# Performance work log

Hardware: AMD Instinct MI355X
Metric: run time of the kernel (lower is better)

Reference implementation:

```python
import jax, jax.numpy as jnp
import numpy as np

N_NODES = 50000
N_EDGES = 800000
IN_DIM = 128
HID_DIM = 64
OUT_DIM = 64
NUM_GRAPHS = 512


def setup_inputs() -> dict:
    key = jax.random.key(0)
    ks = jax.random.split(key, 8)
    x = jax.random.normal(ks[0], (N_NODES, IN_DIM), dtype=jnp.float32)
    edge_index = jax.random.randint(ks[1], (2, N_EDGES), 0, N_NODES, dtype=jnp.int64)
    batch = jnp.sort(jax.random.randint(ks[2], (N_NODES,), 0, NUM_GRAPHS, dtype=jnp.int64))
    s1 = 1.0 / np.sqrt(IN_DIM)
    s2 = 1.0 / np.sqrt(HID_DIM)
    W1 = jax.random.uniform(ks[3], (IN_DIM, HID_DIM), jnp.float32, -s1, s1)
    b1 = jax.random.uniform(ks[4], (HID_DIM,), jnp.float32, -s1, s1)
    W2 = jax.random.uniform(ks[5], (HID_DIM, OUT_DIM), jnp.float32, -s2, s2)
    b2 = jax.random.uniform(ks[6], (OUT_DIM,), jnp.float32, -s2, s2)
    return {"x": x, "edge_index": edge_index, "batch": batch,
            "W1": W1, "b1": b1, "W2": W2, "b2": b2}


def _gcn_layer(h, W, b, src, dst, norm, n_nodes):
    # linear transform first (keeps the per-edge gather at output width)
    h = h @ W + b                      # [N, d_out]
    msg = h[src] * norm[:, None]       # [E, d_out] gathered, normalized messages
    agg = jax.ops.segment_sum(msg, dst, num_segments=n_nodes)  # scatter-add
    return jax.nn.relu(agg)


def reference(x, edge_index, batch, W1, b1, W2, b2):
    src, dst = edge_index[0], edge_index[1]
    # symmetric degree normalization: deg^{-1/2}[src] * deg^{-1/2}[dst]
    deg = jax.ops.segment_sum(jnp.ones((src.shape[0],), x.dtype), dst,
                              num_segments=N_NODES)
    dinv = jax.lax.rsqrt(jnp.maximum(deg, 1.0))
    norm = dinv[src] * dinv[dst]       # [E]

    h = _gcn_layer(x, W1, b1, src, dst, norm, N_NODES)   # dropout = identity (eval)
    h = _gcn_layer(h, W2, b2, src, dst, norm, N_NODES)

    # scatter_mean pooling over batch indices
    sums = jax.ops.segment_sum(h, batch, num_segments=NUM_GRAPHS)
    cnts = jax.ops.segment_sum(jnp.ones((N_NODES,), h.dtype), batch,
                               num_segments=NUM_GRAPHS)
    return sums / jnp.maximum(cnts, 1.0)[:, None]        # [NUM_GRAPHS, OUT_DIM]
```

## Files before the change

kernel.cpp:

```cpp
#include <hip/hip_runtime.h>
#include <hip/hip_fp16.h>

#define N_NODES 50000
#define N_EDGES 800000
#define IN_DIM 128
#define NUM_GRAPHS 512
#define CAP 64
#define NB 196
#define BCAP 5120
#define FILL_T 2048
#define NFILL 391
#define GEMM_TILES 1563

typedef unsigned short u16;
typedef unsigned int u32;

__device__ __forceinline__ void acc_row(const uint4& v, float2& aa, float2& ab,
                                        float2& ac, float2& ad) {
    const __half2* hp = reinterpret_cast<const __half2*>(&v);
    float2 f;
    f = __half22float2(hp[0]); aa.x += f.x; aa.y += f.y;
    f = __half22float2(hp[1]); ab.x += f.x; ab.y += f.y;
    f = __half22float2(hp[2]); ac.x += f.x; ac.y += f.y;
    f = __half22float2(hp[3]); ad.x += f.x; ad.y += f.y;
}

__device__ __forceinline__ void gather_node(
    const uint4* __restrict__ H16, const u16* __restrict__ sp, int dg, int lo,
    float2& aa, float2& ab, float2& ac, float2& ad) {
    int i = 0;
    for (; i + 7 < dg; i += 8) {
        ushort4 s4a = *reinterpret_cast<const ushort4*>(sp + i);
        ushort4 s4b = *reinterpret_cast<const ushort4*>(sp + i + 4);
        uint4 v0 = H16[(size_t)s4a.x * 8 + lo];
        uint4 v1 = H16[(size_t)s4a.y * 8 + lo];
        uint4 v2 = H16[(size_t)s4a.z * 8 + lo];
        uint4 v3 = H16[(size_t)s4a.w * 8 + lo];
        uint4 v4 = H16[(size_t)s4b.x * 8 + lo];
        uint4 v5 = H16[(size_t)s4b.y * 8 + lo];
        uint4 v6 = H16[(size_t)s4b.z * 8 + lo];
        uint4 v7 = H16[(size_t)s4b.w * 8 + lo];
        acc_row(v0, aa, ab, ac, ad); acc_row(v1, aa, ab, ac, ad);
        acc_row(v2, aa, ab, ac, ad); acc_row(v3, aa, ab, ac, ad);
        acc_row(v4, aa, ab, ac, ad); acc_row(v5, aa, ab, ac, ad);
        acc_row(v6, aa, ab, ac, ad); acc_row(v7, aa, ab, ac, ad);
    }
    for (; i + 3 < dg; i += 4) {
        ushort4 s4 = *reinterpret_cast<const ushort4*>(sp + i);
        uint4 v0 = H16[(size_t)s4.x * 8 + lo];
        uint4 v1 = H16[(size_t)s4.y * 8 + lo];
        uint4 v2 = H16[(size_t)s4.z * 8 + lo];
        uint4 v3 = H16[(size_t)s4.w * 8 + lo];
        acc_row(v0, aa, ab, ac, ad); acc_row(v1, aa, ab, ac, ad);
        acc_row(v2, aa, ab, ac, ad); acc_row(v3, aa, ab, ac, ad);
    }
    for (; i < dg; ++i) {
        uint4 v = H16[(size_t)sp[i] * 8 + lo];
        acc_row(v, aa, ab, ac, ad);
    }
}

__global__ __launch_bounds__(256) void gemm1_fill_kernel(
    const float* __restrict__ X, const float* __restrict__ W,
    const float* __restrict__ bias, __half* __restrict__ Yh, int n_nodes,
    const int* __restrict__ src, const int* __restrict__ dst,
    int* __restrict__ gcursor, u32* __restrict__ packed, int n_edges) {
    __shared__ float xs[32][IN_DIM];
    __shared__ int hist[256], cnt2[256], goffs[256];
    const int tid = threadIdx.x;

    if (blockIdx.x & 1) {
        const int fb = blockIdx.x >> 1;
        if (fb >= NFILL) return;
        hist[tid] = 0; cnt2[tid] = 0;
        __syncthreads();
        const int base = fb * FILL_T;
        int d[8], s[8];
#pragma unroll
        for (int i = 0; i < 8; ++i) {
            int e = base + i * 256 + tid;
            if (e < n_edges) {
                d[i] = dst[e]; s[i] = src[e];
                atomicAdd(&hist[d[i] >> 8], 1);
            } else d[i] = -1;
        }
        __syncthreads();
        if (hist[tid] > 0) goffs[tid] = atomicAdd(&gcursor[tid], hist[tid]);
        __syncthreads();
#pragma unroll
        for (int i = 0; i < 8; ++i) {
            if (d[i] >= 0) {
                int b = d[i] >> 8;
                int p = goffs[b] + atomicAdd(&cnt2[b], 1);
                packed[(size_t)b * BCAP + p] = ((u32)d[i] << 16) | (u32)s[i];
            }
        }
        return;
    }

    const int idx = blockIdx.x >> 1;
    if (idx >= GEMM_TILES) return;
    const int base = idx * 32;
    const int nvec = 32 * IN_DIM / 4;
    const float4* X4 = reinterpret_cast<const float4*>(X + (size_t)base * IN_DIM);
    float4* xs4 = reinterpret_cast<float4*>(&xs[0][0]);
    for (int i = tid; i < nvec; i += 256) {
        int row = i / (IN_DIM / 4);
        xs4[i] = (base + row < n_nodes) ? X4[i] : make_float4(0.f, 0.f, 0.f, 0.f);
    }
    __syncthreads();

    const int j = tid & 63;
    const int w = tid >> 6;
    float b = bias[j];
    float c[8];
#pragma unroll
    for (int r = 0; r < 8; ++r) c[r] = b;
#pragma unroll 4
    for (int k = 0; k < IN_DIM; ++k) {
        float wv = W[k * 64 + j];
#pragma unroll
        for (int r = 0; r < 8; ++r) c[r] += wv * xs[w * 8 + r][k];
    }
    int n0 = base + w * 8;
#pragma unroll
    for (int r = 0; r < 8; ++r)
        if (n0 + r < n_nodes)
            Yh[(size_t)(n0 + r) * 64 + j] = __float2half(c[r]);
}

__global__ __launch_bounds__(256) void fine_kernel(
    const u32* __restrict__ packed, const int* __restrict__ gcursor,
    u16* __restrict__ ssorted, int* __restrict__ deg, float* __restrict__ dinv,
    __half* __restrict__ H1h,
    const int* __restrict__ batch, int* __restrict__ gstart, int n_graphs) {
    __shared__ u16 image[128 * CAP];
    __shared__ int cur[128];
    __shared__ float ds[128];
    const int tid = threadIdx.x;

    if (blockIdx.x == 2 * NB) {
        for (int g = tid; g <= n_graphs; g += 256) {
            int lo = 0, hi = N_NODES;
            while (lo < hi) {
                int mid = (lo + hi) >> 1;
                if (batch[mid] < g) lo = mid + 1; else hi = mid;
            }
            gstart[g] = lo;
        }
        return;
    }

    const int b = blockIdx.x >> 1;
    const int half = blockIdx.x & 1;
    if (tid < 128) cur[tid] = 0;
    __syncthreads();
    const int cnt = gcursor[b];
    const u32* pp = packed + (size_t)b * BCAP;
    for (int i = tid; i < cnt; i += 256) {
        u32 p = pp[i];
        int dl = (p >> 16) & 255;
        if ((dl >> 7) == half) {
            int loc = dl & 127;
            int pos = atomicAdd(&cur[loc], 1);
            if (pos < CAP) image[loc * CAP + pos] = (u16)(p & 0xffff);
        }
    }
    __syncthreads();
    const int nbase = b * 256 + half * 128;
    if (tid < 128) {
        int c = cur[tid];
        float dv = rsqrtf(fmaxf((float)c, 1.0f));
        ds[tid] = dv;
        int d = nbase + tid;
        if (d < N_NODES) { deg[d] = c; dinv[d] = dv; }
    }
    __syncthreads();
    const u32* im32 = reinterpret_cast<const u32*>(image);
    u32* out32 = reinterpret_cast<u32*>(ssorted) + (size_t)nbase * (CAP / 2);
    for (int i = tid; i < 128 * CAP / 2; i += 256) out32[i] = im32[i];
    __half2* Hp = reinterpret_cast<__half2*>(H1h) + (size_t)nbase * 32;
    const int lim = min(128, N_NODES - nbase) * 32;
    for (int i = tid; i < lim; i += 256) {
        float dv = ds[i >> 5];
        float2 f = __half22float2(Hp[i]);
        Hp[i] = __floats2half2_rn(f.x * dv, f.y * dv);
    }
}

__global__ __launch_bounds__(256) void agg_gemm_kernel(
    const __half* __restrict__ H, const u16* __restrict__ ssorted,
    const int* __restrict__ deg, const float* __restrict__ dinv,
    const float* __restrict__ W, const float* __restrict__ bias,
    __half* __restrict__ Yh, int n_nodes) {
    __shared__ float xs[32][64];
    const int tid = threadIdx.x;
    const int lane = tid & 63;
    const int w = tid >> 6;
    const int lo = lane & 7;
    const int slot = w * 8 + (lane >> 3);
    const int base = blockIdx.x * 32;
    const uint4* H16 = reinterpret_cast<const uint4*>(H);

    int node = base + slot;
    float2 aa = make_float2(0.f, 0.f), ab = make_float2(0.f, 0.f);
    float2 ac = make_float2(0.f, 0.f), ad = make_float2(0.f, 0.f);
    if (node < n_nodes) {
        int dg = min(deg[node], CAP);
        gather_node(H16, ssorted + (size_t)node * CAP, dg, lo, aa, ab, ac, ad);
        float dv = dinv[node];
        *reinterpret_cast<float4*>(&xs[slot][8 * lo]) =
            make_float4(fmaxf(aa.x * dv, 0.f), fmaxf(aa.y * dv, 0.f),
                        fmaxf(ab.x * dv, 0.f), fmaxf(ab.y * dv, 0.f));
        *reinterpret_cast<float4*>(&xs[slot][8 * lo + 4]) =
            make_float4(fmaxf(ac.x * dv, 0.f), fmaxf(ac.y * dv, 0.f),
                        fmaxf(ad.x * dv, 0.f), fmaxf(ad.y * dv, 0.f));
    } else {
        *reinterpret_cast<float4*>(&xs[slot][8 * lo]) = make_float4(0.f, 0.f, 0.f, 0.f);
        *reinterpret_cast<float4*>(&xs[slot][8 * lo + 4]) = make_float4(0.f, 0.f, 0.f, 0.f);
    }
    __syncthreads();

    float b = bias[lane];
    float c[8];
#pragma unroll
    for (int r = 0; r < 8; ++r) c[r] = b;
#pragma unroll 4
    for (int k = 0; k < 64; ++k) {
        float wv = W[k * 64 + lane];
#pragma unroll
        for (int r = 0; r < 8; ++r) c[r] += wv * xs[w * 8 + r][k];
    }
    int n0 = base + w * 8;
#pragma unroll
    for (int r = 0; r < 8; ++r)
        if (n0 + r < n_nodes)
            Yh[(size_t)(n0 + r) * 64 + lane] = __float2half(c[r] * dinv[n0 + r]);
}

__global__ __launch_bounds__(512) void agg2_pool_kernel(
    const __half* __restrict__ H, const u16* __restrict__ ssorted,
    const int* __restrict__ deg, const float* __restrict__ dinv,
    const int* __restrict__ gstart, float* __restrict__ out) {
    __shared__ float part[64][64];
    const int g = blockIdx.x;
    const int tid = threadIdx.x;
    const int lane = tid & 63;
    const int w = tid >> 6;
    const int lo = lane & 7;
    const int slot = w * 8 + (lane >> 3);
    const uint4* H16 = reinterpret_cast<const uint4*>(H);
    const int beg = gstart[g], end = gstart[g + 1];

    float2 pa = make_float2(0.f, 0.f), pb = make_float2(0.f, 0.f);
    float2 pc = make_float2(0.f, 0.f), pd = make_float2(0.f, 0.f);
    for (int node = beg + slot; node < end; node += 64) {
        int dg = min(deg[node], CAP);
        float2 aa = make_float2(0.f, 0.f), ab = make_float2(0.f, 0.f);
        float2 ac = make_float2(0.f, 0.f), ad = make_float2(0.f, 0.f);
        gather_node(H16, ssorted + (size_t)node * CAP, dg, lo, aa, ab, ac, ad);
        float dv = dinv[node];
        pa.x += fmaxf(aa.x * dv, 0.f); pa.y += fmaxf(aa.y * dv, 0.f);
        pb.x += fmaxf(ab.x * dv, 0.f); pb.y += fmaxf(ab.y * dv, 0.f);
        pc.x += fmaxf(ac.x * dv, 0.f); pc.y += fmaxf(ac.y * dv, 0.f);
        pd.x += fmaxf(ad.x * dv, 0.f); pd.y += fmaxf(ad.y * dv, 0.f);
    }
    *reinterpret_cast<float4*>(&part[slot][8 * lo]) = make_float4(pa.x, pa.y, pb.x, pb.y);
    *reinterpret_cast<float4*>(&part[slot][8 * lo + 4]) = make_float4(pc.x, pc.y, pd.x, pd.y);
    __syncthreads();
    if (tid < 64) {
        float s = 0.f;
#pragma unroll
        for (int r = 0; r < 64; ++r) s += part[r][tid];
        out[(size_t)g * 64 + tid] = s / fmaxf((float)(end - beg), 1.0f);
    }
}

extern "C" void kernel_launch(void* const* d_in, const int* in_sizes, int n_in,
                              void* d_out, int out_size, void* d_ws, size_t ws_size,
                              hipStream_t stream) {
    const float* x     = (const float*)d_in[0];
    const int*   ei    = (const int*)d_in[1];
    const int*   batch = (const int*)d_in[2];
    const float* W1    = (const float*)d_in[3];
    const float* b1    = (const float*)d_in[4];
    const float* W2    = (const float*)d_in[5];
    const float* b2    = (const float*)d_in[6];
    float* out = (float*)d_out;

    const int* srcp = ei;
    const int* dstp = ei + N_EDGES;

    __half* H1h     = (__half*)d_ws;
    __half* H2h     = H1h + (size_t)N_NODES * 64;
    float*  dinv    = (float*)(H2h + (size_t)N_NODES * 64);
    int*    deg     = (int*)(dinv + N_NODES);
    u16*    ssorted = (u16*)(deg + N_NODES);
    u32*    packed  = (u32*)(ssorted + (size_t)NB * 256 * CAP);
    int*    gcursor = (int*)(packed + (size_t)NB * BCAP);
    int*    gstart  = gcursor + 256;

    hipMemsetAsync(gcursor, 0, 256 * sizeof(int), stream);

    gemm1_fill_kernel<<<2 * GEMM_TILES, 256, 0, stream>>>(
        x, W1, b1, H1h, N_NODES, srcp, dstp, gcursor, packed, N_EDGES);

    fine_kernel<<<2 * NB + 1, 256, 0, stream>>>(
        packed, gcursor, ssorted, deg, dinv, H1h, batch, gstart, NUM_GRAPHS);

    agg_gemm_kernel<<<GEMM_TILES, 256, 0, stream>>>(
        H1h, ssorted, deg, dinv, W2, b2, H2h, N_NODES);

    agg2_pool_kernel<<<NUM_GRAPHS, 512, 0, stream>>>(
        H2h, ssorted, deg, dinv, gstart, out);
}
```

Baseline: 172.1 us.

## Register-tile first GEMM with 128-row blocks and shared-memory W chunks

Rewrites the X@W1 part of the fused gemm+fill kernel so each block computes 128 rows instead of 32. Each thread accumulates a 4x8 register tile, X is staged transposed in shared memory and W in 32-row chunks. Output is written as packed 16-byte half vectors. The grid shrinks to match the 391 fill blocks, which cuts block count and redundant W reads, at the cost of more registers and more k-chunk syncs per block.

```diff
diff --git a/kernel.cpp b/kernel.cpp
--- a/kernel.cpp
+++ b/kernel.cpp
@@ -10,6 +10,7 @@
 #define BCAP 5120
 #define FILL_T 2048
 #define NFILL 391
+#define GEMM1_BLKS 391
 #define GEMM_TILES 1563
 
 typedef unsigned short u16;
@@ -65,7 +66,8 @@
     const float* __restrict__ bias, __half* __restrict__ Yh, int n_nodes,
     const int* __restrict__ src, const int* __restrict__ dst,
     int* __restrict__ gcursor, u32* __restrict__ packed, int n_edges) {
-    __shared__ float xs[32][IN_DIM];
+    __shared__ float xst[32][128];
+    __shared__ float ws[32][64];
     __shared__ int hist[256], cnt2[256], goffs[256];
     const int tid = threadIdx.x;
 
@@ -99,34 +101,72 @@
     }
 
     const int idx = blockIdx.x >> 1;
-    if (idx >= GEMM_TILES) return;
-    const int base = idx * 32;
-    const int nvec = 32 * IN_DIM / 4;
-    const float4* X4 = reinterpret_cast<const float4*>(X + (size_t)base * IN_DIM);
-    float4* xs4 = reinterpret_cast<float4*>(&xs[0][0]);
-    for (int i = tid; i < nvec; i += 256) {
-        int row = i / (IN_DIM / 4);
-        xs4[i] = (base + row < n_nodes) ? X4[i] : make_float4(0.f, 0.f, 0.f, 0.f);
-    }
-    __syncthreads();
-
-    const int j = tid & 63;
+    const int base = idx * 128;
+    const int lane = tid & 63;
     const int w = tid >> 6;
-    float b = bias[j];
-    float c[8];
-#pragma unroll
-    for (int r = 0; r < 8; ++r) c[r] = b;
-#pragma unroll 4
-    for (int k = 0; k < IN_DIM; ++k) {
-        float wv = W[k * 64 + j];
-#pragma unroll
-        for (int r = 0; r < 8; ++r) c[r] += wv * xs[w * 8 + r][k];
-    }
-    int n0 = base + w * 8;
-#pragma unroll
-    for (int r = 0; r < 8; ++r)
-        if (n0 + r < n_nodes)
-            Yh[(size_t)(n0 + r) * 64 + j] = __float2half(c[r]);
+    const int jo = lane & 7;
+    const int rg = lane >> 3;
+    const int rowb = w * 32 + rg * 4;
+
+    float cc[4][8];
+    {
+        float4 ba = *reinterpret_cast<const float4*>(bias + jo * 8);
+        float4 bb = *reinterpret_cast<const float4*>(bias + jo * 8 + 4);
+#pragma unroll
+        for (int r = 0; r < 4; ++r) {
+            cc[r][0] = ba.x; cc[r][1] = ba.y; cc[r][2] = ba.z; cc[r][3] = ba.w;
+            cc[r][4] = bb.x; cc[r][5] = bb.y; cc[r][6] = bb.z; cc[r][7] = bb.w;
+        }
+    }
+    const float4* X4 = reinterpret_cast<const float4*>(X);
+    const float4* W4 = reinterpret_cast<const float4*>(W);
+    float4* ws4 = reinterpret_cast<float4*>(&ws[0][0]);
+
+    for (int kc = 0; kc < 4; ++kc) {
+        if (kc) __syncthreads();
+#pragma unroll
+        for (int t = 0; t < 4; ++t) {
+            int i = t * 256 + tid;
+            int row = i >> 3, f4 = i & 7;
+            float4 v = make_float4(0.f, 0.f, 0.f, 0.f);
+            if (base + row < n_nodes) v = X4[(size_t)(base + row) * 32 + kc * 8 + f4];
+            int k0 = f4 * 4;
+            xst[k0 + 0][row] = v.x; xst[k0 + 1][row] = v.y;
+            xst[k0 + 2][row] = v.z; xst[k0 + 3][row] = v.w;
+        }
+#pragma unroll
+        for (int t = 0; t < 2; ++t)
+            ws4[t * 256 + tid] = W4[kc * 512 + t * 256 + tid];
+        __syncthreads();
+
+#pragma unroll 8
+        for (int kk = 0; kk < 32; ++kk) {
+            float4 xv = *reinterpret_cast<const float4*>(&xst[kk][rowb]);
+            float4 wa = *reinterpret_cast<const float4*>(&ws[kk][jo * 8]);
+            float4 wb = *reinterpret_cast<const float4*>(&ws[kk][jo * 8 + 4]);
+            float xr[4] = {xv.x, xv.y, xv.z, xv.w};
+            float wv[8] = {wa.x, wa.y, wa.z, wa.w, wb.x, wb.y, wb.z, wb.w};
+#pragma unroll
+            for (int r = 0; r < 4; ++r)
+#pragma unroll
+                for (int j = 0; j < 8; ++j) cc[r][j] += xr[r] * wv[j];
+        }
+    }
+
+#pragma unroll
+    for (int r = 0; r < 4; ++r) {
+        int row = base + rowb + r;
+        if (row < n_nodes) {
+            __half2 h0 = __floats2half2_rn(cc[r][0], cc[r][1]);
+            __half2 h1 = __floats2half2_rn(cc[r][2], cc[r][3]);
+            __half2 h2 = __floats2half2_rn(cc[r][4], cc[r][5]);
+            __half2 h3 = __floats2half2_rn(cc[r][6], cc[r][7]);
+            uint4 o;
+            o.x = *reinterpret_cast<u32*>(&h0); o.y = *reinterpret_cast<u32*>(&h1);
+            o.z = *reinterpret_cast<u32*>(&h2); o.w = *reinterpret_cast<u32*>(&h3);
+            *reinterpret_cast<uint4*>(Yh + (size_t)row * 64 + jo * 8) = o;
+        }
+    }
 }
 
 __global__ __launch_bounds__(256) void fine_kernel(
@@ -302,7 +342,7 @@
 
     hipMemsetAsync(gcursor, 0, 256 * sizeof(int), stream);
 
-    gemm1_fill_kernel<<<2 * GEMM_TILES, 256, 0, stream>>>(
+    gemm1_fill_kernel<<<2 * NFILL, 256, 0, stream>>>(
         x, W1, b1, H1h, N_NODES, srcp, dstp, gcursor, packed, N_EDGES);
 
     fine_kernel<<<2 * NB + 1, 256, 0, stream>>>(
```

Result: no change. 171.4 us (-0.5%).
